# Optimization experiments

Measured on AMD Instinct MI355X. Metric: run time of the kernel, lower is better.

Reference implementation:

```python
import jax, jax.numpy as jnp
from jax import lax
import numpy as np

D = 8        # domain_num
L = 12       # label_num
C = 9        # attr_num
W = 128      # window_size
B = 4096
EPS = 1e-5


def setup_inputs() -> dict:
    key = jax.random.key(0)
    ks = jax.random.split(key, 12)
    s = 0.05
    return {
        "x": jax.random.normal(ks[0], (B, C, 1, W), dtype=jnp.float32),
        "weights": jax.random.uniform(ks[1], (B, D), dtype=jnp.float32),
        # per-domain stacked parameters (leading dim D)
        "gamma": jnp.ones((D, C), dtype=jnp.float32),
        "beta": jnp.zeros((D, C), dtype=jnp.float32),
        "w1": jax.random.normal(ks[2], (D, 32, C, 9), dtype=jnp.float32) * s,
        "b1": jax.random.normal(ks[3], (D, 32), dtype=jnp.float32) * s,
        "w2": jax.random.normal(ks[4], (D, 64, 32, 9), dtype=jnp.float32) * s,
        "b2": jax.random.normal(ks[5], (D, 64), dtype=jnp.float32) * s,
        "fcw": jax.random.normal(ks[6], (D, L, 64 * 26), dtype=jnp.float32) * s,
        "fcb": jax.random.normal(ks[7], (D, L), dtype=jnp.float32) * s,
    }


def _maxpool2(h):
    # MaxPool along width, kernel 2 stride 2 (height is 1 and already squeezed)
    b, c, w = h.shape
    return h.reshape(b, c, w // 2, 2).max(axis=-1)


def _branch(x3, gamma, beta, w1, b1, w2, b2, fcw, fcb):
    # x3: [B, C, W]. BatchNorm2d in training mode: batch stats over (N, H, W).
    mean = x3.mean(axis=(0, 2), keepdims=True)
    var = x3.var(axis=(0, 2), keepdims=True)
    xn = (x3 - mean) * lax.rsqrt(var + EPS) * gamma[None, :, None] + beta[None, :, None]
    dn = ('NCH', 'OIH', 'NCH')
    h = lax.conv_general_dilated(xn, w1, (1,), 'VALID', dimension_numbers=dn)
    h = _maxpool2(jax.nn.relu(h + b1[None, :, None]))          # [B,32,60]
    h = lax.conv_general_dilated(h, w2, (1,), 'VALID', dimension_numbers=dn)
    h = _maxpool2(jax.nn.relu(h + b2[None, :, None]))          # [B,64,26]
    flat = h.reshape(h.shape[0], 64 * 26)
    return jax.nn.relu(flat @ fcw.T + fcb)                      # [B,L]


def reference(x, weights, gamma, beta, w1, b1, w2, b2, fcw, fcb):
    x3 = x[:, :, 0, :]  # squeeze height=1 -> [B,C,W]
    per_domain = jax.vmap(_branch, in_axes=(None, 0, 0, 0, 0, 0, 0, 0, 0))(
        x3, gamma, beta, w1, b1, w2, b2, fcw, fcb)              # [D,B,L]
    # vectorized form of the nested python-loop weighted sum over domains
    return jnp.einsum('bd,dbl->bl', weights, per_domain)        # [B,L]
```

## Files before the change

kernel.cpp:

```cpp
#include <hip/hip_runtime.h>
#include <hip/hip_bf16.h>

#define D 8
#define L 12
#define C 9
#define W 128
#define B 4096
#define EPS 1e-5f

typedef __attribute__((ext_vector_type(8))) short v8s;
typedef __attribute__((ext_vector_type(4))) float v4f;

#define OFF_STATS 0
#define OFF_B1E   1152
#define OFF_W1T   1408
#define OFF_W2T   21888
#define OFF_FCWP  95616

#define REGION 2336

__device__ inline unsigned short f2bf(float f) {
    unsigned u = __builtin_bit_cast(unsigned, f);
    u += 0x7FFFu + ((u >> 16) & 1u);
    return (unsigned short)(u >> 16);
}
__device__ inline unsigned pk2(float a, float b) {
    float2 f2; f2.x = a; f2.y = b;
    __hip_bfloat162 h = __float22bfloat162_rn(f2);
    unsigned u; __builtin_memcpy(&u, &h, 4);
    return u;
}

__global__ void stats_repack_kernel(const float* __restrict__ x,
                                    const float* __restrict__ w2,
                                    const float* __restrict__ fcw,
                                    float* __restrict__ ws,
                                    float* __restrict__ out) {
    const int t = threadIdx.x;
    __shared__ float redS[8];
    if (blockIdx.x < 576) {
        const int c = blockIdx.x % 9;
        const int slice = blockIdx.x / 9;
        const int w4 = t & 31, br = t >> 5;
        const float4* x4 = (const float4*)x;
        float s = 0.f, s2 = 0.f;
        for (int b = slice * 8 + br; b < B; b += 64 * 8) {
            float4 v = x4[(size_t)b * 288 + c * 32 + w4];
            s  += v.x + v.y + v.z + v.w;
            s2 += v.x * v.x + v.y * v.y + v.z * v.z + v.w * v.w;
        }
        for (int off = 32; off >= 1; off >>= 1) {
            s  += __shfl_down(s, off);
            s2 += __shfl_down(s2, off);
        }
        if ((t & 63) == 0) { redS[(t >> 6) * 2] = s; redS[(t >> 6) * 2 + 1] = s2; }
        __syncthreads();
        if (t == 0) {
            ws[OFF_STATS + slice * 18 + c]     = redS[0] + redS[2] + redS[4] + redS[6];
            ws[OFF_STATS + slice * 18 + 9 + c] = redS[1] + redS[3] + redS[5] + redS[7];
        }
    } else if (blockIdx.x < 616) {
        const int i0 = blockIdx.x - 576;
        const int d = i0 / 5, part = i0 % 5;
        short* w2t  = (short*)(ws + OFF_W2T);
        short* fcwp = (short*)(ws + OFF_FCWP);
        if (part < 2) {
            for (int i = part * 256 + t; i < 64 * 9 * 32; i += 512) {
                int o = i / 288, r = i % 288, tap = r / 32, ic = r & 31;
                w2t[(size_t)d * 18432 + i] =
                    (short)f2bf(w2[(((size_t)(d * 64 + o)) * 32 + ic) * 9 + tap]);
            }
        } else {
            for (int i = (part - 2) * 256 + t; i < 12 * 1664; i += 768) {
                int l = i / 1664, k = i % 1664, p = k >> 6, o = k & 63;
                fcwp[((size_t)d * 12) * 1664 + i] =
                    (short)f2bf(fcw[((size_t)(d * 12 + l)) * 1664 + o * 26 + p]);
            }
        }
    } else {
        const int base = (blockIdx.x - 616) * 6144;
        float4 z; z.x = z.y = z.z = z.w = 0.f;
        float4* o4 = (float4*)(out + base);
        for (int i = t; i < 1536; i += 256) o4[i] = z;
    }
}

__global__ void fold1_kernel(const float* __restrict__ w1, const float* __restrict__ b1,
                             const float* __restrict__ gamma, const float* __restrict__ beta,
                             float* __restrict__ ws) {
    const int d = blockIdx.x, t = threadIdx.x;
    __shared__ float g[9], bt[9];
    if (t < 64) {
        for (int c = 0; c < 9; c++) {
            float s  = ws[OFF_STATS + t * 18 + c];
            float s2 = ws[OFF_STATS + t * 18 + 9 + c];
            for (int off = 32; off >= 1; off >>= 1) {
                s  += __shfl_down(s, off);
                s2 += __shfl_down(s2, off);
            }
            if (t == 0) {
                const float N = (float)B * (float)W;
                float m  = s / N;
                float vv = s2 / N - m * m;
                float inv = rsqrtf(vv + EPS);
                float gg = gamma[d * 9 + c] * inv;
                g[c] = gg; bt[c] = beta[d * 9 + c] - gg * m;
            }
        }
    }
    __syncthreads();
    const int o = t >> 3, sub = t & 7;
    short* w1t = (short*)(ws + OFF_W1T);
    short* dst = w1t + (size_t)d * 5120 + o * 160;
    const float* src = w1 + ((size_t)(d * 32 + o)) * 81;
    float bias_part = 0.f;
    for (int tap = sub; tap < 10; tap += 8) {
        for (int c = 0; c < 16; c++) {
            float v = 0.f;
            if (tap < 9 && c < 9) {
                float wv = src[c * 9 + tap];
                v = wv * g[c];
                bias_part += wv * bt[c];
            }
            dst[tap * 16 + c] = (short)f2bf(v);
        }
    }
    bias_part += __shfl_xor(bias_part, 1);
    bias_part += __shfl_xor(bias_part, 2);
    bias_part += __shfl_xor(bias_part, 4);
    if (sub == 0) ws[OFF_B1E + d * 32 + o] = b1[d * 32 + o] + bias_part;
}

__global__ __launch_bounds__(256, 4)
void branch_kernel(const float* __restrict__ x,
                   const float* __restrict__ b2g,
                   const float* __restrict__ fcb,
                   const float* __restrict__ wts,
                   const float* __restrict__ ws,
                   float* __restrict__ out) {
    const int t = threadIdx.x;
    const int lane = t & 63;
    const int wv = t >> 6;
    const int d = blockIdx.y;
    const int b0 = blockIdx.x * 4;
    const short* w1t  = (const short*)(ws + OFF_W1T) + (size_t)d * 5120;
    const short* w2t  = (const short*)(ws + OFF_W2T) + (size_t)d * 18432;
    const short* fcwp = (const short*)(ws + OFF_FCWP) + (size_t)d * 12 * 1664;
    const float* b1e  = ws + OFF_B1E + d * 32;

    __shared__ __align__(16) short lds[4 * REGION];
    short* myr = &lds[wv * REGION];

    const int n = lane & 15, quad = lane >> 4;

    {
        const float* xrow = x + (size_t)(b0 + wv) * 1152;
        #pragma unroll
        for (int rep = 0; rep < 2; rep++) {
            const int w = lane + rep * 64;
            float v[9];
            #pragma unroll
            for (int c = 0; c < 9; c++) v[c] = xrow[c * 128 + w];
            uint4 lo, hi;
            lo.x = pk2(v[0], v[1]); lo.y = pk2(v[2], v[3]);
            lo.z = pk2(v[4], v[5]); lo.w = pk2(v[6], v[7]);
            hi.x = (unsigned)(unsigned short)f2bf(v[8]); hi.y = 0; hi.z = 0; hi.w = 0;
            *(uint4*)&myr[(0 * 144 + w) * 8] = lo;
            *(uint4*)&myr[(1 * 144 + w) * 8] = hi;
        }
        if (lane < 16) {
            uint4 z; z.x = z.y = z.z = z.w = 0;
            *(uint4*)&myr[(0 * 144 + 128 + lane) * 8] = z;
            *(uint4*)&myr[(1 * 144 + 128 + lane) * 8] = z;
        }
    }

    {
        const int qh = quad >> 1, ql = quad & 1;
        const float bias0 = b1e[n], bias1 = b1e[16 + n];
        v4f acc[8][2];
        #pragma unroll
        for (int mt = 0; mt < 8; mt++)
            #pragma unroll
            for (int nt = 0; nt < 2; nt++) { v4f z = {0.f,0.f,0.f,0.f}; acc[mt][nt] = z; }
        #pragma unroll
        for (int s = 0; s < 5; s++) {
            v8s Bw0 = *(const v8s*)&w1t[n * 160 + (2 * s + qh) * 16 + ql * 8];
            v8s Bw1 = *(const v8s*)&w1t[(16 + n) * 160 + (2 * s + qh) * 16 + ql * 8];
            #pragma unroll
            for (int mt = 0; mt < 8; mt++) {
                const int row = mt * 16 + n + 2 * s + qh;
                v8s Af = *(const v8s*)&myr[(ql * 144 + row) * 8];
                acc[mt][0] = __builtin_amdgcn_mfma_f32_16x16x32_bf16(Af, Bw0, acc[mt][0], 0, 0, 0);
                acc[mt][1] = __builtin_amdgcn_mfma_f32_16x16x32_bf16(Af, Bw1, acc[mt][1], 0, 0, 0);
            }
        }
        unsigned held[16];
        #pragma unroll
        for (int mt = 0; mt < 8; mt++)
            #pragma unroll
            for (int nt = 0; nt < 2; nt++) {
                const float bb = nt ? bias1 : bias0;
                float h0  = fmaxf(fmaxf(acc[mt][nt][0], acc[mt][nt][1]) + bb, 0.f);
                float h1v = fmaxf(fmaxf(acc[mt][nt][2], acc[mt][nt][3]) + bb, 0.f);
                held[mt * 2 + nt] = pk2(h0, h1v);
            }
        #pragma unroll
        for (int mt = 0; mt < 8; mt++) {
            const int p = mt * 8 + quad * 2;
            #pragma unroll
            for (int nt = 0; nt < 2; nt++) {
                const unsigned pr = held[mt * 2 + nt];
                const int plane = nt * 2 + (n >> 3);
                const int col = n & 7;
                if (p < 60)     myr[(plane * 73 + p) * 8 + col]     = (short)(pr & 0xFFFFu);
                if (p + 1 < 60) myr[(plane * 73 + p + 1) * 8 + col] = (short)(pr >> 16);
            }
        }
    }

    {
        float biasv[4];
        #pragma unroll
        for (int nt = 0; nt < 4; nt++) biasv[nt] = b2g[d * 64 + nt * 16 + n];
        v4f acc[4][4];
        #pragma unroll
        for (int mt = 0; mt < 4; mt++)
            #pragma unroll
            for (int nt = 0; nt < 4; nt++) { v4f z = {0.f,0.f,0.f,0.f}; acc[mt][nt] = z; }
        for (int tap = 0; tap < 9; tap++) {
            v8s Bw[4];
            #pragma unroll
            for (int nt = 0; nt < 4; nt++)
                Bw[nt] = *(const v8s*)&w2t[(nt * 16 + n) * 288 + tap * 32 + quad * 8];
            #pragma unroll
            for (int mt = 0; mt < 4; mt++) {
                const int row = mt * 16 + n + tap;
                v8s Af = *(const v8s*)&myr[(quad * 73 + row) * 8];
                #pragma unroll
                for (int nt = 0; nt < 4; nt++)
                    acc[mt][nt] = __builtin_amdgcn_mfma_f32_16x16x32_bf16(Af, Bw[nt], acc[mt][nt], 0, 0, 0);
            }
        }
        unsigned held[16];
        #pragma unroll
        for (int mt = 0; mt < 4; mt++)
            #pragma unroll
            for (int nt = 0; nt < 4; nt++) {
                float h0  = fmaxf(fmaxf(acc[mt][nt][0], acc[mt][nt][1]) + biasv[nt], 0.f);
                float h1v = fmaxf(fmaxf(acc[mt][nt][2], acc[mt][nt][3]) + biasv[nt], 0.f);
                held[mt * 4 + nt] = pk2(h0, h1v);
            }
        #pragma unroll
        for (int mt = 0; mt < 4; mt++) {
            const int p = mt * 8 + quad * 2;
            #pragma unroll
            for (int nt = 0; nt < 4; nt++) {
                const unsigned pr = held[mt * 4 + nt];
                const int oc = nt * 16 + n;
                if (p < 26) {
                    const int gs = (oc >> 3) ^ (p & 7);
                    myr[p * 64 + gs * 8 + (oc & 7)] = (short)(pr & 0xFFFFu);
                }
                if (p + 1 < 26) {
                    const int gs = (oc >> 3) ^ ((p + 1) & 7);
                    myr[(p + 1) * 64 + gs * 8 + (oc & 7)] = (short)(pr >> 16);
                }
            }
        }
    }
    __syncthreads();

    {
        const int lrow = (n < 12) ? n : 0;
        v4f acc = {0.f, 0.f, 0.f, 0.f};
        for (int ks = wv; ks < 52; ks += 4) {
            const int p = ks >> 1;
            const int gs = ((ks & 1) * 4 + quad) ^ (p & 7);
            v8s A  = *(const v8s*)&fcwp[lrow * 1664 + ks * 32 + quad * 8];
            v8s Bf = *(const v8s*)&lds[(n & 3) * REGION + p * 64 + gs * 8];
            acc = __builtin_amdgcn_mfma_f32_16x16x32_bf16(A, Bf, acc, 0, 0, 0);
        }
        float* red = (float*)(myr + 1672);
        *(float4*)&red[lane * 4] = *(float4*)&acc;
    }
    __syncthreads();
    if (t < 64) {
        float sum[4] = {0.f, 0.f, 0.f, 0.f};
        #pragma unroll
        for (int w = 0; w < 4; w++) {
            const float* redw = (const float*)(&lds[w * REGION + 1672]);
            float4 v = *(const float4*)&redw[lane * 4];
            sum[0] += v.x; sum[1] += v.y; sum[2] += v.z; sum[3] += v.w;
        }
        if (n < 4) {
            const float wgt = wts[(size_t)(b0 + n) * 8 + d];
            #pragma unroll
            for (int r = 0; r < 4; r++) {
                const int l = quad * 4 + r;
                if (l < 12) {
                    float v = fmaxf(sum[r] + fcb[d * 12 + l], 0.f);
                    atomicAdd(&out[(size_t)(b0 + n) * 12 + l], wgt * v);
                }
            }
        }
    }
}

extern "C" void kernel_launch(void* const* d_in, const int* in_sizes, int n_in,
                              void* d_out, int out_size, void* d_ws, size_t ws_size,
                              hipStream_t stream) {
    const float* x       = (const float*)d_in[0];
    const float* weights = (const float*)d_in[1];
    const float* gamma   = (const float*)d_in[2];
    const float* beta    = (const float*)d_in[3];
    const float* w1      = (const float*)d_in[4];
    const float* b1      = (const float*)d_in[5];
    const float* w2      = (const float*)d_in[6];
    const float* b2      = (const float*)d_in[7];
    const float* fcw     = (const float*)d_in[8];
    const float* fcb     = (const float*)d_in[9];
    float* ws  = (float*)d_ws;
    float* out = (float*)d_out;

    stats_repack_kernel<<<dim3(624), 256, 0, stream>>>(x, w2, fcw, ws, out);
    fold1_kernel<<<dim3(D), 256, 0, stream>>>(w1, b1, gamma, beta, ws);
    branch_kernel<<<dim3(B / 4, D), 256, 0, stream>>>(x, b2, fcb, weights, ws, out);
}
```

Measured before the change: 236.0 us.

## Pre-pack x to bf16 once in stats pass and DMA it into LDS per branch

```diff
diff --git a/kernel.cpp b/kernel.cpp
--- a/kernel.cpp
+++ b/kernel.cpp
@@ -12,10 +12,12 @@
 typedef __attribute__((ext_vector_type(4))) float v4f;
 
 #define OFF_STATS 0
-#define OFF_B1E   1152
-#define OFF_W1T   1408
-#define OFF_W2T   21888
-#define OFF_FCWP  95616
+#define OFF_B1E   18432
+#define OFF_W1T   18688
+#define OFF_W2T   39168
+#define OFF_FCWP  112896
+#define OFF_XG    192768
+#define WS_XG_FLOATS (OFF_XG + (B * 2304) / 2)
 
 #define REGION 2336
 
@@ -30,55 +32,97 @@
     unsigned u; __builtin_memcpy(&u, &h, 4);
     return u;
 }
+__device__ inline void gl_lds16(const void* g, void* l) {
+    __builtin_amdgcn_global_load_lds(
+        (const __attribute__((address_space(1))) void*)g,
+        (__attribute__((address_space(3))) void*)l, 16, 0, 0);
+}
+__device__ inline void gl_lds4(const void* g, void* l) {
+    __builtin_amdgcn_global_load_lds(
+        (const __attribute__((address_space(1))) void*)g,
+        (__attribute__((address_space(3))) void*)l, 4, 0, 0);
+}
 
 __global__ void stats_repack_kernel(const float* __restrict__ x,
                                     const float* __restrict__ w2,
                                     const float* __restrict__ fcw,
                                     float* __restrict__ ws,
-                                    float* __restrict__ out) {
+                                    float* __restrict__ out,
+                                    int use_xg) {
     const int t = threadIdx.x;
-    __shared__ float redS[8];
-    if (blockIdx.x < 576) {
-        const int c = blockIdx.x % 9;
-        const int slice = blockIdx.x / 9;
-        const int w4 = t & 31, br = t >> 5;
-        const float4* x4 = (const float4*)x;
-        float s = 0.f, s2 = 0.f;
-        for (int b = slice * 8 + br; b < B; b += 64 * 8) {
-            float4 v = x4[(size_t)b * 288 + c * 32 + w4];
-            s  += v.x + v.y + v.z + v.w;
-            s2 += v.x * v.x + v.y * v.y + v.z * v.z + v.w * v.w;
-        }
-        for (int off = 32; off >= 1; off >>= 1) {
-            s  += __shfl_down(s, off);
-            s2 += __shfl_down(s2, off);
-        }
-        if ((t & 63) == 0) { redS[(t >> 6) * 2] = s; redS[(t >> 6) * 2 + 1] = s2; }
+    __shared__ float red2[4][18];
+    if (blockIdx.x < 1024) {
+        const int rb = blockIdx.x * 4;
+        const int w = t & 127, half = t >> 7;
+        float s[9], s2[9];
+        #pragma unroll
+        for (int c = 0; c < 9; c++) { s[c] = 0.f; s2[c] = 0.f; }
+        #pragma unroll
+        for (int pass = 0; pass < 2; pass++) {
+            const int row = rb + pass * 2 + half;
+            const float* xr = x + (size_t)row * 1152 + w;
+            float v[9];
+            #pragma unroll
+            for (int c = 0; c < 9; c++) {
+                v[c] = xr[c * 128];
+                s[c] += v[c]; s2[c] += v[c] * v[c];
+            }
+            if (use_xg) {
+                short* xgr = (short*)(ws + OFF_XG) + (size_t)row * 2304;
+                uint4 lo, hi;
+                lo.x = pk2(v[0], v[1]); lo.y = pk2(v[2], v[3]);
+                lo.z = pk2(v[4], v[5]); lo.w = pk2(v[6], v[7]);
+                hi.x = (unsigned)(unsigned short)f2bf(v[8]); hi.y = 0; hi.z = 0; hi.w = 0;
+                *(uint4*)&xgr[w * 8] = lo;
+                *(uint4*)&xgr[(144 + w) * 8] = hi;
+            }
+        }
+        if (use_xg && t < 128) {
+            const int row = rb + (t >> 5), j = t & 31;
+            uint4 z; z.x = z.y = z.z = z.w = 0;
+            *(uint4*)&((short*)(ws + OFF_XG))[(size_t)row * 2304 +
+                                              ((j >> 4) * 144 + 128 + (j & 15)) * 8] = z;
+        }
+        #pragma unroll
+        for (int c = 0; c < 9; c++) {
+            #pragma unroll
+            for (int off = 32; off >= 1; off >>= 1) {
+                s[c]  += __shfl_down(s[c], off);
+                s2[c] += __shfl_down(s2[c], off);
+            }
+        }
+        if ((t & 63) == 0) {
+            #pragma unroll
+            for (int c = 0; c < 9; c++) {
+                red2[t >> 6][c] = s[c]; red2[t >> 6][9 + c] = s2[c];
+            }
+        }
         __syncthreads();
-        if (t == 0) {
-            ws[OFF_STATS + slice * 18 + c]     = redS[0] + redS[2] + redS[4] + redS[6];
-            ws[OFF_STATS + slice * 18 + 9 + c] = redS[1] + redS[3] + redS[5] + redS[7];
-        }
-    } else if (blockIdx.x < 616) {
-        const int i0 = blockIdx.x - 576;
-        const int d = i0 / 5, part = i0 % 5;
-        short* w2t  = (short*)(ws + OFF_W2T);
-        short* fcwp = (short*)(ws + OFF_FCWP);
-        if (part < 2) {
-            for (int i = part * 256 + t; i < 64 * 9 * 32; i += 512) {
-                int o = i / 288, r = i % 288, tap = r / 32, ic = r & 31;
-                w2t[(size_t)d * 18432 + i] =
-                    (short)f2bf(w2[(((size_t)(d * 64 + o)) * 32 + ic) * 9 + tap]);
-            }
-        } else {
-            for (int i = (part - 2) * 256 + t; i < 12 * 1664; i += 768) {
-                int l = i / 1664, k = i % 1664, p = k >> 6, o = k & 63;
-                fcwp[((size_t)d * 12) * 1664 + i] =
-                    (short)f2bf(fcw[((size_t)(d * 12 + l)) * 1664 + o * 26 + p]);
-            }
+        if (t < 18)
+            ws[OFF_STATS + t * 1024 + blockIdx.x] =
+                red2[0][t] + red2[1][t] + red2[2][t] + red2[3][t];
+    } else if (blockIdx.x < 1152) {
+        const int g = (blockIdx.x - 1024) * 4 + (t >> 6);
+        const int lane = t & 63;
+        const int d = g >> 6, o = g & 63;
+        const float* src = w2 + (size_t)(d * 64 + o) * 288;
+        short* dst = (short*)(ws + OFF_W2T) + (size_t)d * 18432 + o * 288;
+        for (int i = lane; i < 288; i += 64) {
+            int ic = i / 9, tap = i % 9;
+            dst[tap * 32 + ic] = (short)f2bf(src[i]);
+        }
+    } else if (blockIdx.x < 1200) {
+        const int g = (blockIdx.x - 1152) * 4 + (t >> 6);
+        const int lane = t & 63;
+        const int dl = g >> 1, half = g & 1;
+        const float* src = fcw + (size_t)dl * 1664;
+        short* dst = (short*)(ws + OFF_FCWP) + (size_t)dl * 1664;
+        for (int i = half * 832 + lane; i < half * 832 + 832; i += 64) {
+            int o = i / 26, p = i % 26;
+            dst[p * 64 + o] = (short)f2bf(src[i]);
         }
     } else {
-        const int base = (blockIdx.x - 616) * 6144;
+        const int base = (blockIdx.x - 1200) * 6144;
         float4 z; z.x = z.y = z.z = z.w = 0.f;
         float4* o4 = (float4*)(out + base);
         for (int i = t; i < 1536; i += 256) o4[i] = z;
@@ -89,26 +133,34 @@
                              const float* __restrict__ gamma, const float* __restrict__ beta,
                              float* __restrict__ ws) {
     const int d = blockIdx.x, t = threadIdx.x;
+    __shared__ float redA[8];
     __shared__ float g[9], bt[9];
-    if (t < 64) {
-        for (int c = 0; c < 9; c++) {
-            float s  = ws[OFF_STATS + t * 18 + c];
-            float s2 = ws[OFF_STATS + t * 18 + 9 + c];
-            for (int off = 32; off >= 1; off >>= 1) {
-                s  += __shfl_down(s, off);
-                s2 += __shfl_down(s2, off);
-            }
-            if (t == 0) {
-                const float N = (float)B * (float)W;
-                float m  = s / N;
-                float vv = s2 / N - m * m;
-                float inv = rsqrtf(vv + EPS);
-                float gg = gamma[d * 9 + c] * inv;
-                g[c] = gg; bt[c] = beta[d * 9 + c] - gg * m;
-            }
-        }
-    }
-    __syncthreads();
+    for (int c = 0; c < 9; c++) {
+        float s = 0.f, s2 = 0.f;
+        #pragma unroll
+        for (int j = 0; j < 4; j++) {
+            s  += ws[OFF_STATS + c * 1024 + t + 256 * j];
+            s2 += ws[OFF_STATS + (9 + c) * 1024 + t + 256 * j];
+        }
+        #pragma unroll
+        for (int off = 32; off >= 1; off >>= 1) {
+            s  += __shfl_down(s, off);
+            s2 += __shfl_down(s2, off);
+        }
+        if ((t & 63) == 0) { redA[(t >> 6) * 2] = s; redA[(t >> 6) * 2 + 1] = s2; }
+        __syncthreads();
+        if (t == 0) {
+            float st  = redA[0] + redA[2] + redA[4] + redA[6];
+            float st2 = redA[1] + redA[3] + redA[5] + redA[7];
+            const float N = (float)B * (float)W;
+            float m  = st / N;
+            float vv = st2 / N - m * m;
+            float inv = rsqrtf(vv + EPS);
+            float gg = gamma[d * 9 + c] * inv;
+            g[c] = gg; bt[c] = beta[d * 9 + c] - gg * m;
+        }
+        __syncthreads();
+    }
     const int o = t >> 3, sub = t & 7;
     short* w1t = (short*)(ws + OFF_W1T);
     short* dst = w1t + (size_t)d * 5120 + o * 160;
@@ -131,6 +183,7 @@
     if (sub == 0) ws[OFF_B1E + d * 32 + o] = b1[d * 32 + o] + bias_part;
 }
 
+template<bool XG>
 __global__ __launch_bounds__(256, 4)
 void branch_kernel(const float* __restrict__ x,
                    const float* __restrict__ b2g,
@@ -153,7 +206,16 @@
 
     const int n = lane & 15, quad = lane >> 4;
 
-    {
+    if (XG) {
+        const char* xgrow = (const char*)(ws + OFF_XG) + (size_t)(b0 + wv) * 4608;
+        char* lb = (char*)myr;
+        #pragma unroll
+        for (int k = 0; k < 4; k++)
+            gl_lds16(xgrow + k * 1024 + lane * 16, lb + k * 1024);
+        gl_lds4(xgrow + 4096 + lane * 4, lb + 4096);
+        gl_lds4(xgrow + 4352 + lane * 4, lb + 4352);
+        asm volatile("s_waitcnt vmcnt(0)" ::: "memory");
+    } else {
         const float* xrow = x + (size_t)(b0 + wv) * 1152;
         #pragma unroll
         for (int rep = 0; rep < 2; rep++) {
@@ -323,7 +385,12 @@
     float* ws  = (float*)d_ws;
     float* out = (float*)d_out;
 
-    stats_repack_kernel<<<dim3(624), 256, 0, stream>>>(x, w2, fcw, ws, out);
+    const int use_xg = (ws_size >= (size_t)WS_XG_FLOATS * 4) ? 1 : 0;
+
+    stats_repack_kernel<<<dim3(1208), 256, 0, stream>>>(x, w2, fcw, ws, out, use_xg);
     fold1_kernel<<<dim3(D), 256, 0, stream>>>(w1, b1, gamma, beta, ws);
-    branch_kernel<<<dim3(B / 4, D), 256, 0, stream>>>(x, b2, fcb, weights, ws, out);
-}
+    if (use_xg)
+        branch_kernel<true><<<dim3(B / 4, D), 256, 0, stream>>>(x, b2, fcb, weights, ws, out);
+    else
+        branch_kernel<false><<<dim3(B / 4, D), 256, 0, stream>>>(x, b2, fcb, weights, ws, out);
+}
```

New measurement: 248.7 us. 1.05x slower.
